# Optimization experiments

Hardware: AMD Instinct MI355X
Metric: run time of the kernel (lower is better)

The kernel has to match this reference:

```python
import jax, jax.numpy as jnp
import numpy as np

N = 50000   # nodes
E = 800000  # edges
D = 128     # att_dim
H = 8       # heads
DH = D // H # head dim
EPS = 1e-5


def _ln(x, g, b):
    m = jnp.mean(x, axis=-1, keepdims=True)
    v = jnp.mean((x - m) ** 2, axis=-1, keepdims=True)
    return (x - m) * jax.lax.rsqrt(v + EPS) * g + b


def setup_inputs() -> dict:
    key = jax.random.key(0)
    ks = jax.random.split(key, 12)
    s = 1.0 / np.sqrt(D)
    w = lambda k, sh: (jax.random.normal(k, sh, jnp.float32) * s)
    return {
        'x': jax.random.normal(ks[0], (N, D), jnp.float32),
        'idx_i': jax.random.randint(ks[1], (E,), 0, N, jnp.int32),
        'idx_j': jax.random.randint(ks[2], (E,), 0, N, jnp.int32),
        'Wq': w(ks[3], (D, D)), 'bq': jnp.zeros((D,), jnp.float32),
        'Wk': w(ks[4], (D, D)), 'bk': jnp.zeros((D,), jnp.float32),
        'Wv': w(ks[5], (D, D)), 'bv': jnp.zeros((D,), jnp.float32),
        'Wo': w(ks[6], (D, D)), 'bo': jnp.zeros((D,), jnp.float32),
        'g1': jnp.ones((D,), jnp.float32), 'be1': jnp.zeros((D,), jnp.float32),
        'W1': w(ks[7], (D, D)), 'bb1': jnp.zeros((D,), jnp.float32),
        'W2': w(ks[8], (D, D)), 'bb2': jnp.zeros((D,), jnp.float32),
        'g2': jnp.ones((D,), jnp.float32), 'be2': jnp.zeros((D,), jnp.float32),
    }


def reference(x, idx_i, idx_j, Wq, bq, Wk, bk, Wv, bv, Wo, bo,
              g1, be1, W1, bb1, W2, bb2, g2, be2):
    # --- EdgeAttentionLayer: multi-head dot-product attention over edges ---
    q = (x @ Wq + bq).reshape(N, H, DH)   # n h d
    k = (x @ Wk + bk).reshape(N, H, DH)
    v = (x @ Wv + bv).reshape(N, H, DH)
    q_i = q[idx_i]                         # (E, H, DH) gather at destination
    k_j = k[idx_j]                         # (E, H, DH) gather at source
    e = jnp.einsum('ehd,ehd->eh', q_i, k_j) / np.sqrt(DH)  # (E, H)
    # segment softmax over edges sharing the same destination node idx_i
    m = jax.ops.segment_max(e, idx_i, num_segments=N)       # (N, H)
    a = jnp.exp(e - m[idx_i])
    denom = jax.ops.segment_sum(a, idx_i, num_segments=N)   # (N, H)
    alpha = a / denom[idx_i]                                 # (E, H)
    agg = jax.ops.segment_sum(alpha[:, :, None] * v[idx_j], idx_i,
                              num_segments=N)                # (N, H, DH)
    x1 = agg.reshape(N, D) @ Wo + bo
    # --- residual + LayerNorm ---
    h = _ln(x + x1, g1, be1)
    # --- ResLayer projection: Linear -> ReLU -> Linear, residual, LayerNorm ---
    y = jax.nn.relu(h @ W1 + bb1) @ W2 + bb2
    return _ln(h + y, g2, be2)
```

## Files before the change

kernel.cpp:

```cpp
#include <hip/hip_runtime.h>
#include <hip/hip_bf16.h>
#include <math.h>

#define D 128
#define H 8
#define DH 16
#define SCAN_CHUNK 1024

typedef __attribute__((ext_vector_type(8))) short bf16x8;
typedef __attribute__((ext_vector_type(4))) float f32x4;

__device__ __forceinline__ float bf2f(ushort u) {
    unsigned int x = ((unsigned int)u) << 16;
    float f;
    __builtin_memcpy(&f, &x, 4);
    return f;
}
__device__ __forceinline__ ushort f2bf(float f) {
    __hip_bfloat16 h = __float2bfloat16(f);
    ushort u;
    __builtin_memcpy(&u, &h, 2);
    return u;
}

#define STAGE_W(SRC, LDSBUF)                                              \
    {                                                                      \
        _Pragma("unroll")                                                  \
        for (int it_ = 0; it_ < 8; ++it_) {                                \
            int idx16_ = t + it_ * 256;                                    \
            int row_ = idx16_ >> 4, c16_ = idx16_ & 15;                    \
            int d_ = (row_ << 7) + ((c16_ ^ (row_ & 7)) << 3);             \
            *(bf16x8*)((LDSBUF) + d_) = *(const bf16x8*)((SRC) + idx16_ * 8); \
        }                                                                  \
    }

#define WOFF(rn, kk) (((rn) << 7) + ((((l4) + (kk) * 4) ^ ((rn) & 7)) << 3))

#define LOAD_A(SRCH, SRCL, BASE, AH, AL)                                   \
    _Pragma("unroll")                                                      \
    for (int kk_ = 0; kk_ < 4; ++kk_) {                                    \
        AH[kk_] = *(const bf16x8*)((SRCH) + (BASE) + kk_ * 32);            \
        AL[kk_] = *(const bf16x8*)((SRCL) + (BASE) + kk_ * 32);            \
    }

#define TILE_MFMA(AH0, AL0, AH1, AL1, WH, WL, ACC0, ACC1)                  \
    _Pragma("unroll")                                                      \
    for (int kk = 0; kk < 4; ++kk) {                                       \
        _Pragma("unroll")                                                  \
        for (int n = 0; n < 8; ++n) {                                      \
            int rn = n * 16 + l15;                                         \
            bf16x8 bh = *(const bf16x8*)((WH) + WOFF(rn, kk));             \
            bf16x8 bl = *(const bf16x8*)((WL) + WOFF(rn, kk));             \
            ACC0[n] = __builtin_amdgcn_mfma_f32_16x16x32_bf16(AH0[kk], bh, ACC0[n], 0, 0, 0); \
            ACC0[n] = __builtin_amdgcn_mfma_f32_16x16x32_bf16(AL0[kk], bh, ACC0[n], 0, 0, 0); \
            ACC0[n] = __builtin_amdgcn_mfma_f32_16x16x32_bf16(AH0[kk], bl, ACC0[n], 0, 0, 0); \
            ACC1[n] = __builtin_amdgcn_mfma_f32_16x16x32_bf16(AH1[kk], bh, ACC1[n], 0, 0, 0); \
            ACC1[n] = __builtin_amdgcn_mfma_f32_16x16x32_bf16(AL1[kk], bh, ACC1[n], 0, 0, 0); \
            ACC1[n] = __builtin_amdgcn_mfma_f32_16x16x32_bf16(AH1[kk], bl, ACC1[n], 0, 0, 0); \
        }                                                                  \
    }


__global__ __launch_bounds__(256) void zero_kernel(int* __restrict__ count, int n) {
    int gid = blockIdx.x * blockDim.x + threadIdx.x;
    if (gid < n) count[gid] = 0;
}


__global__ __launch_bounds__(256) void prep_x_kernel(
    const float* __restrict__ x, ushort* __restrict__ xh, ushort* __restrict__ xl,
    int total4)
{
    int gid = blockIdx.x * blockDim.x + threadIdx.x;
    if (gid >= total4) return;
    float4 v = ((const float4*)x)[gid];
    ushort4 hv, lv;
    hv.x = f2bf(v.x); lv.x = f2bf(v.x - bf2f(hv.x));
    hv.y = f2bf(v.y); lv.y = f2bf(v.y - bf2f(hv.y));
    hv.z = f2bf(v.z); lv.z = f2bf(v.z - bf2f(hv.z));
    hv.w = f2bf(v.w); lv.w = f2bf(v.w - bf2f(hv.w));
    ((ushort4*)xh)[gid] = hv;
    ((ushort4*)xl)[gid] = lv;
}


__global__ __launch_bounds__(256) void prep_w_kernel(
    const float* __restrict__ w0, const float* __restrict__ w1,
    const float* __restrict__ w2, const float* __restrict__ w3,
    const float* __restrict__ w4, const float* __restrict__ w5,
    ushort* __restrict__ wth, ushort* __restrict__ wtl)
{
    __shared__ __align__(16) float tile[128][132];
    const int m = blockIdx.x;
    const float* W = (m == 0) ? w0 : (m == 1) ? w1 : (m == 2) ? w2
                   : (m == 3) ? w3 : (m == 4) ? w4 : w5;
    const int t = threadIdx.x;
    const float4* wg = (const float4*)W;
    #pragma unroll
    for (int it = 0; it < 16; ++it) {
        int f4 = t + it * 256;
        int k = f4 >> 5, c4 = f4 & 31;
        *((float4*)&tile[k][c4 * 4]) = wg[f4];
    }
    __syncthreads();
    ushort* oh = wth + m * 16384;
    ushort* ol = wtl + m * 16384;
    #pragma unroll
    for (int it = 0; it < 64; ++it) {
        int idx = t + it * 256;
        int c = idx >> 7, k = idx & 127;
        float v = tile[k][c];
        ushort hb = f2bf(v);
        oh[idx] = hb;
        ol[idx] = f2bf(v - bf2f(hb));
    }
}


__global__ __launch_bounds__(256) void gemm_qkv_kernel(
    const ushort* __restrict__ xh, const ushort* __restrict__ xl,
    const ushort* __restrict__ wth, const ushort* __restrict__ wtl,
    const float* __restrict__ bq, const float* __restrict__ bk,
    const float* __restrict__ bv,
    float* __restrict__ q, ushort* __restrict__ k16, ushort* __restrict__ v16,
    int n_rows)
{
    __shared__ __align__(16) ushort wh[16384];
    __shared__ __align__(16) ushort wl[16384];
    const int t = threadIdx.x;
    const int w = t >> 6, l = t & 63;
    const int l15 = l & 15, l4 = l >> 4;
    const int m = blockIdx.y;

    STAGE_W(wth + m * 16384, wh);
    STAGE_W(wtl + m * 16384, wl);

    const float* bias = (m == 0) ? bq : (m == 1) ? bk : bv;
    float bsv[8];
    #pragma unroll
    for (int n = 0; n < 8; ++n) bsv[n] = bias[n * 16 + l15];
    __syncthreads();

    const int ntiles = (n_rows + 127) >> 7;
    for (int tile = blockIdx.x; tile < ntiles; tile += gridDim.x) {
        const int rowb = tile * 128 + w * 32;
        const size_t a0 = (size_t)(rowb + l15) * D + l4 * 8;
        bf16x8 ah0[4], al0[4], ah1[4], al1[4];
        LOAD_A(xh, xl, a0, ah0, al0);
        LOAD_A(xh, xl, a0 + 16 * D, ah1, al1);
        f32x4 acc0[8], acc1[8];
        #pragma unroll
        for (int n = 0; n < 8; ++n) {
            acc0[n] = (f32x4){0.f, 0.f, 0.f, 0.f};
            acc1[n] = (f32x4){0.f, 0.f, 0.f, 0.f};
        }
        TILE_MFMA(ah0, al0, ah1, al1, wh, wl, acc0, acc1);
        #pragma unroll
        for (int n = 0; n < 8; ++n) {
            int col = n * 16 + l15;
            #pragma unroll
            for (int r = 0; r < 4; ++r) {
                int row0 = rowb + l4 * 4 + r;
                int row1 = row0 + 16;
                if (row0 < n_rows) {
                    float val = acc0[n][r] + bsv[n];
                    if (m == 0) q[(size_t)row0 * D + col] = val;
                    else if (m == 1) k16[(size_t)row0 * D + col] = f2bf(val);
                    else v16[(size_t)row0 * D + col] = f2bf(val);
                }
                if (row1 < n_rows) {
                    float val = acc1[n][r] + bsv[n];
                    if (m == 0) q[(size_t)row1 * D + col] = val;
                    else if (m == 1) k16[(size_t)row1 * D + col] = f2bf(val);
                    else v16[(size_t)row1 * D + col] = f2bf(val);
                }
            }
        }
    }
}


__global__ __launch_bounds__(256) void hist_kernel(
    const int* __restrict__ idx_i, int* __restrict__ count, int n_edges)
{
    int e = blockIdx.x * blockDim.x + threadIdx.x;
    if (e < n_edges) atomicAdd(&count[idx_i[e]], 1);
}

__global__ __launch_bounds__(256) void scan_reduce_kernel(
    const int* __restrict__ count, int* __restrict__ bsum, int n)
{
    __shared__ int wsum[4];
    const int t = threadIdx.x, lane = t & 63, w = t >> 6;
    int base = blockIdx.x * SCAN_CHUNK + t * 4;
    int s = 0;
    #pragma unroll
    for (int i = 0; i < 4; ++i) {
        int idx = base + i;
        if (idx < n) s += count[idx];
    }
    #pragma unroll
    for (int off = 1; off < 64; off <<= 1) s += __shfl_xor(s, off);
    if (lane == 0) wsum[w] = s;
    __syncthreads();
    if (t == 0) bsum[blockIdx.x] = wsum[0] + wsum[1] + wsum[2] + wsum[3];
}

__global__ __launch_bounds__(64) void scan_bsum_kernel(
    int* __restrict__ bsum, int* __restrict__ row_start, int nb, int n)
{
    const int t = threadIdx.x;
    int iv = (t < nb) ? bsum[t] : 0;
    int vv = iv;
    #pragma unroll
    for (int off = 1; off < 64; off <<= 1) {
        int u = __shfl_up(vv, off);
        if (t >= off) vv += u;
    }
    if (t < nb) bsum[t] = vv - iv;
    if (t == 63) row_start[n] = vv;
}

__global__ __launch_bounds__(256) void scan_write_kernel(
    const int* __restrict__ count, const int* __restrict__ bsum,
    int* __restrict__ row_start, int* __restrict__ cursor, int n)
{
    __shared__ int wtot[4];
    const int t = threadIdx.x, lane = t & 63, w = t >> 6;
    int base = blockIdx.x * SCAN_CHUNK + t * 4;
    int c0 = 0, c1 = 0, c2 = 0, c3 = 0;
    if (base + 0 < n) c0 = count[base + 0];
    if (base + 1 < n) c1 = count[base + 1];
    if (base + 2 < n) c2 = count[base + 2];
    if (base + 3 < n) c3 = count[base + 3];
    int tsum = c0 + c1 + c2 + c3;
    int inc = tsum;
    #pragma unroll
    for (int off = 1; off < 64; off <<= 1) {
        int u = __shfl_up(inc, off);
        if (lane >= off) inc += u;
    }
    if (lane == 63) wtot[w] = inc;
    __syncthreads();
    int wb = 0;
    for (int i = 0; i < w; ++i) wb += wtot[i];
    int start = bsum[blockIdx.x] + wb + inc - tsum;
    if (base + 0 < n) { row_start[base + 0] = start;            cursor[base + 0] = start; }
    if (base + 1 < n) { row_start[base + 1] = start + c0;       cursor[base + 1] = start + c0; }
    if (base + 2 < n) { row_start[base + 2] = start + c0 + c1;  cursor[base + 2] = start + c0 + c1; }
    if (base + 3 < n) { row_start[base + 3] = start + c0 + c1 + c2; cursor[base + 3] = start + c0 + c1 + c2; }
}

__global__ __launch_bounds__(256) void scatter_kernel(
    const int* __restrict__ idx_i, const int* __restrict__ idx_j,
    int* __restrict__ cursor, int* __restrict__ ejs, int n_edges)
{
    int e = blockIdx.x * blockDim.x + threadIdx.x;
    if (e < n_edges) {
        int i = idx_i[e];
        int pos = atomicAdd(&cursor[i], 1);
        ejs[pos] = idx_j[e];
    }
}


__global__ __launch_bounds__(256) void fused_agg_kernel(
    const float* __restrict__ q, const ushort* __restrict__ k16,
    const ushort* __restrict__ v16, const int* __restrict__ row_start,
    const int* __restrict__ ejs,
    ushort* __restrict__ aggh, ushort* __restrict__ aggl, int n_nodes)
{
    const int lane = threadIdx.x & 63;
    const int node = (blockIdx.x * blockDim.x + threadIdx.x) >> 6;
    if (node >= n_nodes) return;
    const int beg = row_start[node], end = row_start[node + 1];
    const int half = lane >> 5, sl = lane & 31;
    const int c4 = sl * 4;

    if (beg >= end) {
        if (half == 0) {
            ((uint2*)(aggh + (size_t)node * D))[sl] = make_uint2(0u, 0u);
            ((uint2*)(aggl + (size_t)node * D))[sl] = make_uint2(0u, 0u);
        }
        return;
    }

    const float4 qv = *(const float4*)&q[(size_t)node * D + c4];
    const float SC = 0.25f * 1.4426950408889634f;
    float m = -INFINITY, l = 0.f;
    float a0 = 0.f, a1 = 0.f, a2 = 0.f, a3 = 0.f;

    int p = beg + half;
    uint2 kr0, vr0, kr1, vr1;
    if (p < end) {
        int j = ejs[p];
        kr0 = *(const uint2*)(k16 + (size_t)j * D + c4);
        vr0 = *(const uint2*)(v16 + (size_t)j * D + c4);
    }
    if (p + 2 < end) {
        int j = ejs[p + 2];
        kr1 = *(const uint2*)(k16 + (size_t)j * D + c4);
        vr1 = *(const uint2*)(v16 + (size_t)j * D + c4);
    }
    while (p < end) {
        uint2 kc = kr0, vc = vr0;
        kr0 = kr1; vr0 = vr1;
        if (p + 4 < end) {
            int j = ejs[p + 4];
            kr1 = *(const uint2*)(k16 + (size_t)j * D + c4);
            vr1 = *(const uint2*)(v16 + (size_t)j * D + c4);
        }
        float k0 = bf2f((ushort)kc.x), k1 = bf2f((ushort)(kc.x >> 16));
        float k2 = bf2f((ushort)kc.y), k3 = bf2f((ushort)(kc.y >> 16));
        float d = qv.x * k0 + qv.y * k1 + qv.z * k2 + qv.w * k3;
        d += __shfl_xor(d, 1);
        d += __shfl_xor(d, 2);
        float s = d * SC;
        float mn = fmaxf(m, s);
        float c  = exp2f(m - mn);
        float pe = exp2f(s - mn);
        float v0 = bf2f((ushort)vc.x), v1 = bf2f((ushort)(vc.x >> 16));
        float v2 = bf2f((ushort)vc.y), v3 = bf2f((ushort)(vc.y >> 16));
        l  = l  * c + pe;
        a0 = a0 * c + pe * v0;
        a1 = a1 * c + pe * v1;
        a2 = a2 * c + pe * v2;
        a3 = a3 * c + pe * v3;
        m = mn;
        p += 2;
    }

    float m2 = __shfl_xor(m, 32);
    float l2 = __shfl_xor(l, 32);
    float b0 = __shfl_xor(a0, 32);
    float b1 = __shfl_xor(a1, 32);
    float b2 = __shfl_xor(a2, 32);
    float b3 = __shfl_xor(a3, 32);
    float mm = fmaxf(m, m2);
    float cA = exp2f(m - mm);
    float cB = exp2f(m2 - mm);
    float L  = l * cA + l2 * cB;
    float A0 = a0 * cA + b0 * cB;
    float A1 = a1 * cA + b1 * cB;
    float A2 = a2 * cA + b2 * cB;
    float A3 = a3 * cA + b3 * cB;
    float invl = (L > 0.f) ? (1.0f / L) : 0.f;
    float o0 = A0 * invl, o1 = A1 * invl, o2 = A2 * invl, o3 = A3 * invl;

    ushort h0 = f2bf(o0), h1 = f2bf(o1), h2 = f2bf(o2), h3 = f2bf(o3);
    if (half == 0) {
        uint2 hv;
        hv.x = (unsigned int)h0 | ((unsigned int)h1 << 16);
        hv.y = (unsigned int)h2 | ((unsigned int)h3 << 16);
        ((uint2*)(aggh + (size_t)node * D))[sl] = hv;
    } else {
        ushort l0 = f2bf(o0 - bf2f(h0)), l1 = f2bf(o1 - bf2f(h1));
        ushort l2_ = f2bf(o2 - bf2f(h2)), l3 = f2bf(o3 - bf2f(h3));
        uint2 lv;
        lv.x = (unsigned int)l0 | ((unsigned int)l1 << 16);
        lv.y = (unsigned int)l2_ | ((unsigned int)l3 << 16);
        ((uint2*)(aggl + (size_t)node * D))[sl] = lv;
    }
}


__global__ __launch_bounds__(256) void gemm_oproj_kernel(
    const ushort* __restrict__ aggh, const ushort* __restrict__ aggl,
    const float* __restrict__ x,
    const ushort* __restrict__ wth, const ushort* __restrict__ wtl,
    const float* __restrict__ bo, const float* __restrict__ g1,
    const float* __restrict__ be1,
    ushort* __restrict__ hh, ushort* __restrict__ hl, int n_rows)
{
    __shared__ __align__(16) ushort wh[16384];
    __shared__ __align__(16) ushort wl[16384];
    const int t = threadIdx.x;
    const int w = t >> 6, l = t & 63;
    const int l15 = l & 15, l4 = l >> 4;

    STAGE_W(wth, wh);
    STAGE_W(wtl, wl);
    float bsv[8], gv[8], bev[8];
    #pragma unroll
    for (int n = 0; n < 8; ++n) {
        int col = n * 16 + l15;
        bsv[n] = bo[col]; gv[n] = g1[col]; bev[n] = be1[col];
    }
    __syncthreads();

    const int ntiles = (n_rows + 127) >> 7;
    for (int tile = blockIdx.x; tile < ntiles; tile += gridDim.x) {
        const int rowb = tile * 128 + w * 32;
        const size_t a0 = (size_t)(rowb + l15) * D + l4 * 8;
        bf16x8 ah0[4], al0[4], ah1[4], al1[4];
        LOAD_A(aggh, aggl, a0, ah0, al0);
        LOAD_A(aggh, aggl, a0 + 16 * D, ah1, al1);
        f32x4 acc0[8], acc1[8];
        #pragma unroll
        for (int n = 0; n < 8; ++n) {
            acc0[n] = (f32x4){0.f, 0.f, 0.f, 0.f};
            acc1[n] = (f32x4){0.f, 0.f, 0.f, 0.f};
        }
        TILE_MFMA(ah0, al0, ah1, al1, wh, wl, acc0, acc1);
        #pragma unroll
        for (int g = 0; g < 2; ++g) {
            f32x4* acc = g ? acc1 : acc0;
            int rbase = rowb + g * 16;
            float vals[8][4];
            #pragma unroll
            for (int n = 0; n < 8; ++n) {
                int col = n * 16 + l15;
                #pragma unroll
                for (int r = 0; r < 4; ++r) {
                    int row = rbase + l4 * 4 + r;
                    float xr = (row < n_rows) ? x[(size_t)row * D + col] : 0.f;
                    vals[n][r] = acc[n][r] + bsv[n] + xr;
                }
            }
            #pragma unroll
            for (int r = 0; r < 4; ++r) {
                int row = rbase + l4 * 4 + r;
                float s = 0.f, ss = 0.f;
                #pragma unroll
                for (int n = 0; n < 8; ++n) { s += vals[n][r]; ss += vals[n][r] * vals[n][r]; }
                #pragma unroll
                for (int msk = 1; msk <= 8; msk <<= 1) {
                    s += __shfl_xor(s, msk);
                    ss += __shfl_xor(ss, msk);
                }
                float mean = s * (1.0f / D);
                float var = ss * (1.0f / D) - mean * mean;
                float inv = rsqrtf(var + 1e-5f);
                if (row < n_rows) {
                    #pragma unroll
                    for (int n = 0; n < 8; ++n) {
                        int col = n * 16 + l15;
                        float y = (vals[n][r] - mean) * inv * gv[n] + bev[n];
                        ushort hb = f2bf(y);
                        hh[(size_t)row * D + col] = hb;
                        hl[(size_t)row * D + col] = f2bf(y - bf2f(hb));
                    }
                }
            }
        }
    }
}


__global__ __launch_bounds__(256) void gemm_ffn1_kernel(
    const ushort* __restrict__ hh, const ushort* __restrict__ hl,
    const ushort* __restrict__ wth, const ushort* __restrict__ wtl,
    const float* __restrict__ bb1,
    ushort* __restrict__ th, ushort* __restrict__ tl, int n_rows)
{
    __shared__ __align__(16) ushort wh[16384];
    __shared__ __align__(16) ushort wl[16384];
    const int t = threadIdx.x;
    const int w = t >> 6, l = t & 63;
    const int l15 = l & 15, l4 = l >> 4;

    STAGE_W(wth, wh);
    STAGE_W(wtl, wl);
    float bsv[8];
    #pragma unroll
    for (int n = 0; n < 8; ++n) bsv[n] = bb1[n * 16 + l15];
    __syncthreads();

    const int ntiles = (n_rows + 127) >> 7;
    for (int tile = blockIdx.x; tile < ntiles; tile += gridDim.x) {
        const int rowb = tile * 128 + w * 32;
        const size_t a0 = (size_t)(rowb + l15) * D + l4 * 8;
        bf16x8 ah0[4], al0[4], ah1[4], al1[4];
        LOAD_A(hh, hl, a0, ah0, al0);
        LOAD_A(hh, hl, a0 + 16 * D, ah1, al1);
        f32x4 acc0[8], acc1[8];
        #pragma unroll
        for (int n = 0; n < 8; ++n) {
            acc0[n] = (f32x4){0.f, 0.f, 0.f, 0.f};
            acc1[n] = (f32x4){0.f, 0.f, 0.f, 0.f};
        }
        TILE_MFMA(ah0, al0, ah1, al1, wh, wl, acc0, acc1);
        #pragma unroll
        for (int n = 0; n < 8; ++n) {
            int col = n * 16 + l15;
            #pragma unroll
            for (int r = 0; r < 4; ++r) {
                int row0 = rowb + l4 * 4 + r;
                int row1 = row0 + 16;
                if (row0 < n_rows) {
                    float tv = fmaxf(acc0[n][r] + bsv[n], 0.f);
                    ushort hb = f2bf(tv);
                    th[(size_t)row0 * D + col] = hb;
                    tl[(size_t)row0 * D + col] = f2bf(tv - bf2f(hb));
                }
                if (row1 < n_rows) {
                    float tv = fmaxf(acc1[n][r] + bsv[n], 0.f);
                    ushort hb = f2bf(tv);
                    th[(size_t)row1 * D + col] = hb;
                    tl[(size_t)row1 * D + col] = f2bf(tv - bf2f(hb));
                }
            }
        }
    }
}


__global__ __launch_bounds__(256) void gemm_ffn2_kernel(
    const ushort* __restrict__ th, const ushort* __restrict__ tl,
    const ushort* __restrict__ hh, const ushort* __restrict__ hl,
    const ushort* __restrict__ wth, const ushort* __restrict__ wtl,
    const float* __restrict__ bb2, const float* __restrict__ g2,
    const float* __restrict__ be2,
    float* __restrict__ out, int n_rows)
{
    __shared__ __align__(16) ushort wh[16384];
    __shared__ __align__(16) ushort wl[16384];
    const int t = threadIdx.x;
    const int w = t >> 6, l = t & 63;
    const int l15 = l & 15, l4 = l >> 4;

    STAGE_W(wth, wh);
    STAGE_W(wtl, wl);
    float bsv[8], gv[8], bev[8];
    #pragma unroll
    for (int n = 0; n < 8; ++n) {
        int col = n * 16 + l15;
        bsv[n] = bb2[col]; gv[n] = g2[col]; bev[n] = be2[col];
    }
    __syncthreads();

    const int ntiles = (n_rows + 127) >> 7;
    for (int tile = blockIdx.x; tile < ntiles; tile += gridDim.x) {
        const int rowb = tile * 128 + w * 32;
        const size_t a0 = (size_t)(rowb + l15) * D + l4 * 8;
        bf16x8 ah0[4], al0[4], ah1[4], al1[4];
        LOAD_A(th, tl, a0, ah0, al0);
        LOAD_A(th, tl, a0 + 16 * D, ah1, al1);
        f32x4 acc0[8], acc1[8];
        #pragma unroll
        for (int n = 0; n < 8; ++n) {
            acc0[n] = (f32x4){0.f, 0.f, 0.f, 0.f};
            acc1[n] = (f32x4){0.f, 0.f, 0.f, 0.f};
        }
        TILE_MFMA(ah0, al0, ah1, al1, wh, wl, acc0, acc1);
        #pragma unroll
        for (int g = 0; g < 2; ++g) {
            f32x4* acc = g ? acc1 : acc0;
            int rbase = rowb + g * 16;
            float vals[8][4];
            #pragma unroll
            for (int n = 0; n < 8; ++n) {
                int col = n * 16 + l15;
                #pragma unroll
                for (int r = 0; r < 4; ++r) {
                    int row = rbase + l4 * 4 + r;
                    float hr = 0.f;
                    if (row < n_rows)
                        hr = bf2f(hh[(size_t)row * D + col]) + bf2f(hl[(size_t)row * D + col]);
                    vals[n][r] = acc[n][r] + bsv[n] + hr;
                }
            }
            #pragma unroll
            for (int r = 0; r < 4; ++r) {
                int row = rbase + l4 * 4 + r;
                float s = 0.f, ss = 0.f;
                #pragma unroll
                for (int n = 0; n < 8; ++n) { s += vals[n][r]; ss += vals[n][r] * vals[n][r]; }
                #pragma unroll
                for (int msk = 1; msk <= 8; msk <<= 1) {
                    s += __shfl_xor(s, msk);
                    ss += __shfl_xor(ss, msk);
                }
                float mean = s * (1.0f / D);
                float var = ss * (1.0f / D) - mean * mean;
                float inv = rsqrtf(var + 1e-5f);
                if (row < n_rows) {
                    #pragma unroll
                    for (int n = 0; n < 8; ++n) {
                        int col = n * 16 + l15;
                        out[(size_t)row * D + col] = (vals[n][r] - mean) * inv * gv[n] + bev[n];
                    }
                }
            }
        }
    }
}


extern "C" void kernel_launch(void* const* d_in, const int* in_sizes, int n_in,
                              void* d_out, int out_size, void* d_ws, size_t ws_size,
                              hipStream_t stream) {
    const float* x     = (const float*)d_in[0];
    const int*   idx_i = (const int*)d_in[1];
    const int*   idx_j = (const int*)d_in[2];
    const float* Wq = (const float*)d_in[3];
    const float* bq = (const float*)d_in[4];
    const float* Wk = (const float*)d_in[5];
    const float* bk = (const float*)d_in[6];
    const float* Wv = (const float*)d_in[7];
    const float* bv = (const float*)d_in[8];
    const float* Wo = (const float*)d_in[9];
    const float* bo = (const float*)d_in[10];
    const float* g1 = (const float*)d_in[11];
    const float* be1 = (const float*)d_in[12];
    const float* W1 = (const float*)d_in[13];
    const float* bb1 = (const float*)d_in[14];
    const float* W2 = (const float*)d_in[15];
    const float* bb2 = (const float*)d_in[16];
    const float* g2 = (const float*)d_in[17];
    const float* be2 = (const float*)d_in[18];

    const int N_ = in_sizes[0] / D;
    const int E_ = in_sizes[1];
    const size_t ND = (size_t)N_ * D;
    const int nb = (N_ + SCAN_CHUNK - 1) / SCAN_CHUNK;

    float* ws = (float*)d_ws;
    float* q = ws;
    ushort* k16 = (ushort*)(q + ND);
    ushort* v16 = k16 + ND;
    int* count     = (int*)(v16 + ND);
    int* row_start = count + N_;
    int* cursor    = row_start + N_ + 1;
    int* bsum      = cursor + N_;
    int* ejs       = bsum + 64;
    ushort* xh = (ushort*)(ejs + E_);
    ushort* xl = xh + ND;
    ushort* wth = xl + ND;
    ushort* wtl = wth + 6 * 16384;
    ushort* aggh = xh;
    ushort* aggl = xl;
    ushort* hh = (ushort*)q;
    ushort* hl = hh + ND;
    ushort* th = k16;
    ushort* tl = v16;

    zero_kernel<<<(N_ + 255) / 256, 256, 0, stream>>>(count, N_);
    prep_x_kernel<<<((int)(ND / 4) + 255) / 256, 256, 0, stream>>>(x, xh, xl, (int)(ND / 4));
    prep_w_kernel<<<6, 256, 0, stream>>>(Wq, Wk, Wv, Wo, W1, W2, wth, wtl);
    {
        dim3 g(171, 3);
        gemm_qkv_kernel<<<g, 256, 0, stream>>>(xh, xl, wth, wtl,
                                               bq, bk, bv, q, k16, v16, N_);
    }
    hist_kernel<<<(E_ + 255) / 256, 256, 0, stream>>>(idx_i, count, E_);
    scan_reduce_kernel<<<nb, 256, 0, stream>>>(count, bsum, N_);
    scan_bsum_kernel<<<1, 64, 0, stream>>>(bsum, row_start, nb, N_);
    scan_write_kernel<<<nb, 256, 0, stream>>>(count, bsum, row_start, cursor, N_);
    scatter_kernel<<<(E_ + 255) / 256, 256, 0, stream>>>(idx_i, idx_j, cursor, ejs, E_);
    fused_agg_kernel<<<(N_ + 3) / 4, 256, 0, stream>>>(q, k16, v16, row_start, ejs,
                                                       aggh, aggl, N_);
    gemm_oproj_kernel<<<196, 256, 0, stream>>>(aggh, aggl, x,
                                               wth + 3 * 16384, wtl + 3 * 16384,
                                               bo, g1, be1, hh, hl, N_);
    gemm_ffn1_kernel<<<196, 256, 0, stream>>>(hh, hl,
                                              wth + 4 * 16384, wtl + 4 * 16384,
                                              bb1, th, tl, N_);
    gemm_ffn2_kernel<<<196, 256, 0, stream>>>(th, tl, hh, hl,
                                              wth + 5 * 16384, wtl + 5 * 16384,
                                              bb2, g2, be2, (float*)d_out, N_);
}
```

Measured before the change: 291.8 us.

## Double-buffer A fragments in GEMMs and add lazy softmax rescaling in aggregation

All four split-bf16 GEMM kernels now prefetch the next tile's A fragments into a second register set while computing the current tile, hiding global load latency. Each also gets __launch_bounds__(256,2), and the QKV grid shrinks from 171 to 131 blocks per matrix. The aggregation kernel pre-scales q and skips the online-softmax rescale unless some lane's score exceeds the running max by more than 8 (log2 units), turning most updates into plain FMAs. The extra fragment registers raise register pressure, and the lazy max lets exponent terms grow by up to 2^8 before rescaling.

Measured after the change: 414.1 us. 41.9% more time.

```diff
diff --git a/kernel.cpp b/kernel.cpp
--- a/kernel.cpp
+++ b/kernel.cpp
@@ -34,31 +34,48 @@
         }                                                                  \
     }
 
-#define WOFF(rn, kk) (((rn) << 7) + ((((l4) + (kk) * 4) ^ ((rn) & 7)) << 3))
-
-#define LOAD_A(SRCH, SRCL, BASE, AH, AL)                                   \
-    _Pragma("unroll")                                                      \
-    for (int kk_ = 0; kk_ < 4; ++kk_) {                                    \
-        AH[kk_] = *(const bf16x8*)((SRCH) + (BASE) + kk_ * 32);            \
-        AL[kk_] = *(const bf16x8*)((SRCL) + (BASE) + kk_ * 32);            \
-    }
-
-#define TILE_MFMA(AH0, AL0, AH1, AL1, WH, WL, ACC0, ACC1)                  \
-    _Pragma("unroll")                                                      \
-    for (int kk = 0; kk < 4; ++kk) {                                       \
+#define DECL_FRAGS(P) bf16x8 P##h0[4], P##l0[4], P##h1[4], P##l1[4]
+
+#define LOAD_FRAGS(SRCH, SRCL, TILE, P)                                    \
+    {                                                                      \
+        const int rb_ = (TILE) * 128 + w * 32;                             \
+        const size_t a0_ = (size_t)(rb_ + l15) * D + l4 * 8;               \
         _Pragma("unroll")                                                  \
-        for (int n = 0; n < 8; ++n) {                                      \
-            int rn = n * 16 + l15;                                         \
-            bf16x8 bh = *(const bf16x8*)((WH) + WOFF(rn, kk));             \
-            bf16x8 bl = *(const bf16x8*)((WL) + WOFF(rn, kk));             \
-            ACC0[n] = __builtin_amdgcn_mfma_f32_16x16x32_bf16(AH0[kk], bh, ACC0[n], 0, 0, 0); \
-            ACC0[n] = __builtin_amdgcn_mfma_f32_16x16x32_bf16(AL0[kk], bh, ACC0[n], 0, 0, 0); \
-            ACC0[n] = __builtin_amdgcn_mfma_f32_16x16x32_bf16(AH0[kk], bl, ACC0[n], 0, 0, 0); \
-            ACC1[n] = __builtin_amdgcn_mfma_f32_16x16x32_bf16(AH1[kk], bh, ACC1[n], 0, 0, 0); \
-            ACC1[n] = __builtin_amdgcn_mfma_f32_16x16x32_bf16(AL1[kk], bh, ACC1[n], 0, 0, 0); \
-            ACC1[n] = __builtin_amdgcn_mfma_f32_16x16x32_bf16(AH1[kk], bl, ACC1[n], 0, 0, 0); \
+        for (int kk_ = 0; kk_ < 4; ++kk_) {                                \
+            P##h0[kk_] = *(const bf16x8*)((SRCH) + a0_ + kk_ * 32);        \
+            P##l0[kk_] = *(const bf16x8*)((SRCL) + a0_ + kk_ * 32);        \
+            P##h1[kk_] = *(const bf16x8*)((SRCH) + a0_ + 16 * D + kk_ * 32); \
+            P##l1[kk_] = *(const bf16x8*)((SRCL) + a0_ + 16 * D + kk_ * 32); \
         }                                                                  \
     }
+
+__device__ __forceinline__ f32x4 MFMA(bf16x8 a, bf16x8 b, f32x4 c) {
+    return __builtin_amdgcn_mfma_f32_16x16x32_bf16(a, b, c, 0, 0, 0);
+}
+
+__device__ __forceinline__ void tile_mfma(
+    const bf16x8* ah0, const bf16x8* al0,
+    const bf16x8* ah1, const bf16x8* al1,
+    const ushort* wh, const ushort* wl, int l15, int l4,
+    f32x4* acc0, f32x4* acc1)
+{
+    #pragma unroll
+    for (int kk = 0; kk < 4; ++kk) {
+        #pragma unroll
+        for (int n = 0; n < 8; ++n) {
+            int rn = n * 16 + l15;
+            int off = (rn << 7) + (((l4 + kk * 4) ^ (rn & 7)) << 3);
+            bf16x8 bh = *(const bf16x8*)(wh + off);
+            bf16x8 bl = *(const bf16x8*)(wl + off);
+            acc0[n] = MFMA(ah0[kk], bh, acc0[n]);
+            acc0[n] = MFMA(al0[kk], bh, acc0[n]);
+            acc0[n] = MFMA(ah0[kk], bl, acc0[n]);
+            acc1[n] = MFMA(ah1[kk], bh, acc1[n]);
+            acc1[n] = MFMA(al1[kk], bh, acc1[n]);
+            acc1[n] = MFMA(ah1[kk], bl, acc1[n]);
+        }
+    }
+}
 
 
 __global__ __launch_bounds__(256) void zero_kernel(int* __restrict__ count, int n) {
@@ -117,7 +134,39 @@
 }
 
 
-__global__ __launch_bounds__(256) void gemm_qkv_kernel(
+#define QKV_ITER(TILE, P)                                                  \
+    {                                                                      \
+        f32x4 acc0[8], acc1[8];                                            \
+        _Pragma("unroll")                                                  \
+        for (int n = 0; n < 8; ++n) {                                      \
+            acc0[n] = (f32x4){0.f, 0.f, 0.f, 0.f};                         \
+            acc1[n] = (f32x4){0.f, 0.f, 0.f, 0.f};                         \
+        }                                                                  \
+        tile_mfma(P##h0, P##l0, P##h1, P##l1, wh, wl, l15, l4, acc0, acc1);\
+        const int rowb_ = (TILE) * 128 + w * 32;                           \
+        _Pragma("unroll")                                                  \
+        for (int n = 0; n < 8; ++n) {                                      \
+            int col = n * 16 + l15;                                        \
+            _Pragma("unroll")                                              \
+            for (int r = 0; r < 4; ++r) {                                  \
+                int row0 = rowb_ + l4 * 4 + r, row1 = row0 + 16;           \
+                if (row0 < n_rows) {                                       \
+                    float val = acc0[n][r] + bsv[n];                       \
+                    if (mat == 0) q[(size_t)row0 * D + col] = val;         \
+                    else if (mat == 1) k16[(size_t)row0 * D + col] = f2bf(val); \
+                    else v16[(size_t)row0 * D + col] = f2bf(val);          \
+                }                                                          \
+                if (row1 < n_rows) {                                       \
+                    float val = acc1[n][r] + bsv[n];                       \
+                    if (mat == 0) q[(size_t)row1 * D + col] = val;         \
+                    else if (mat == 1) k16[(size_t)row1 * D + col] = f2bf(val); \
+                    else v16[(size_t)row1 * D + col] = f2bf(val);          \
+                }                                                          \
+            }                                                              \
+        }                                                                  \
+    }
+
+__global__ __launch_bounds__(256, 2) void gemm_qkv_kernel(
     const ushort* __restrict__ xh, const ushort* __restrict__ xl,
     const ushort* __restrict__ wth, const ushort* __restrict__ wtl,
     const float* __restrict__ bq, const float* __restrict__ bk,
@@ -130,52 +179,34 @@
     const int t = threadIdx.x;
     const int w = t >> 6, l = t & 63;
     const int l15 = l & 15, l4 = l >> 4;
-    const int m = blockIdx.y;
-
-    STAGE_W(wth + m * 16384, wh);
-    STAGE_W(wtl + m * 16384, wl);
-
-    const float* bias = (m == 0) ? bq : (m == 1) ? bk : bv;
+    const int mat = blockIdx.y;
+
+    STAGE_W(wth + mat * 16384, wh);
+    STAGE_W(wtl + mat * 16384, wl);
+    const float* bias = (mat == 0) ? bq : (mat == 1) ? bk : bv;
     float bsv[8];
     #pragma unroll
     for (int n = 0; n < 8; ++n) bsv[n] = bias[n * 16 + l15];
     __syncthreads();
 
     const int ntiles = (n_rows + 127) >> 7;
-    for (int tile = blockIdx.x; tile < ntiles; tile += gridDim.x) {
-        const int rowb = tile * 128 + w * 32;
-        const size_t a0 = (size_t)(rowb + l15) * D + l4 * 8;
-        bf16x8 ah0[4], al0[4], ah1[4], al1[4];
-        LOAD_A(xh, xl, a0, ah0, al0);
-        LOAD_A(xh, xl, a0 + 16 * D, ah1, al1);
-        f32x4 acc0[8], acc1[8];
-        #pragma unroll
-        for (int n = 0; n < 8; ++n) {
-            acc0[n] = (f32x4){0.f, 0.f, 0.f, 0.f};
-            acc1[n] = (f32x4){0.f, 0.f, 0.f, 0.f};
-        }
-        TILE_MFMA(ah0, al0, ah1, al1, wh, wl, acc0, acc1);
-        #pragma unroll
-        for (int n = 0; n < 8; ++n) {
-            int col = n * 16 + l15;
-            #pragma unroll
-            for (int r = 0; r < 4; ++r) {
-                int row0 = rowb + l4 * 4 + r;
-                int row1 = row0 + 16;
-                if (row0 < n_rows) {
-                    float val = acc0[n][r] + bsv[n];
-                    if (m == 0) q[(size_t)row0 * D + col] = val;
-                    else if (m == 1) k16[(size_t)row0 * D + col] = f2bf(val);
-                    else v16[(size_t)row0 * D + col] = f2bf(val);
-                }
-                if (row1 < n_rows) {
-                    float val = acc1[n][r] + bsv[n];
-                    if (m == 0) q[(size_t)row1 * D + col] = val;
-                    else if (m == 1) k16[(size_t)row1 * D + col] = f2bf(val);
-                    else v16[(size_t)row1 * D + col] = f2bf(val);
-                }
-            }
-        }
+    const int g = gridDim.x;
+    int tile = blockIdx.x;
+    if (tile >= ntiles) return;
+
+    DECL_FRAGS(pA);
+    DECL_FRAGS(pB);
+    LOAD_FRAGS(xh, xl, tile, pA);
+    for (;;) {
+        int n1 = tile + g;
+        if (n1 < ntiles) LOAD_FRAGS(xh, xl, n1, pB);
+        QKV_ITER(tile, pA);
+        if (n1 >= ntiles) break;
+        int n2 = n1 + g;
+        if (n2 < ntiles) LOAD_FRAGS(xh, xl, n2, pA);
+        QKV_ITER(n1, pB);
+        if (n2 >= ntiles) break;
+        tile = n2;
     }
 }
 
@@ -285,8 +316,9 @@
         return;
     }
 
-    const float4 qv = *(const float4*)&q[(size_t)node * D + c4];
     const float SC = 0.25f * 1.4426950408889634f;
+    float4 qv = *(const float4*)&q[(size_t)node * D + c4];
+    qv.x *= SC; qv.y *= SC; qv.z *= SC; qv.w *= SC;
     float m = -INFINITY, l = 0.f;
     float a0 = 0.f, a1 = 0.f, a2 = 0.f, a3 = 0.f;
 
@@ -312,21 +344,29 @@
         }
         float k0 = bf2f((ushort)kc.x), k1 = bf2f((ushort)(kc.x >> 16));
         float k2 = bf2f((ushort)kc.y), k3 = bf2f((ushort)(kc.y >> 16));
-        float d = qv.x * k0 + qv.y * k1 + qv.z * k2 + qv.w * k3;
-        d += __shfl_xor(d, 1);
-        d += __shfl_xor(d, 2);
-        float s = d * SC;
-        float mn = fmaxf(m, s);
-        float c  = exp2f(m - mn);
-        float pe = exp2f(s - mn);
+        float s = qv.x * k0 + qv.y * k1 + qv.z * k2 + qv.w * k3;
+        s += __shfl_xor(s, 1);
+        s += __shfl_xor(s, 2);
         float v0 = bf2f((ushort)vc.x), v1 = bf2f((ushort)(vc.x >> 16));
         float v2 = bf2f((ushort)vc.y), v3 = bf2f((ushort)(vc.y >> 16));
-        l  = l  * c + pe;
-        a0 = a0 * c + pe * v0;
-        a1 = a1 * c + pe * v1;
-        a2 = a2 * c + pe * v2;
-        a3 = a3 * c + pe * v3;
-        m = mn;
+        if (__any(s > m + 8.f)) {
+            float mn = fmaxf(m, s);
+            float c  = exp2f(m - mn);
+            float pe = exp2f(s - mn);
+            l  = l  * c + pe;
+            a0 = a0 * c + pe * v0;
+            a1 = a1 * c + pe * v1;
+            a2 = a2 * c + pe * v2;
+            a3 = a3 * c + pe * v3;
+            m = mn;
+        } else {
+            float pe = exp2f(s - m);
+            l += pe;
+            a0 = fmaf(pe, v0, a0);
+            a1 = fmaf(pe, v1, a1);
+            a2 = fmaf(pe, v2, a2);
+            a3 = fmaf(pe, v3, a3);
+        }
         p += 2;
     }
 
@@ -364,7 +404,65 @@
 }
 
 
-__global__ __launch_bounds__(256) void gemm_oproj_kernel(
+__device__ __forceinline__ void oproj_epi(
+    const f32x4* acc, int rbase, int l15, int l4,
+    const float* __restrict__ x, const float* bsv, const float* gv,
+    const float* bev, ushort* __restrict__ hh, ushort* __restrict__ hl,
+    int n_rows)
+{
+    float vals[8][4];
+    #pragma unroll
+    for (int n = 0; n < 8; ++n) {
+        int col = n * 16 + l15;
+        #pragma unroll
+        for (int r = 0; r < 4; ++r) {
+            int row = rbase + l4 * 4 + r;
+            float xr = (row < n_rows) ? x[(size_t)row * D + col] : 0.f;
+            vals[n][r] = acc[n][r] + bsv[n] + xr;
+        }
+    }
+    #pragma unroll
+    for (int r = 0; r < 4; ++r) {
+        int row = rbase + l4 * 4 + r;
+        float s = 0.f, ss = 0.f;
+        #pragma unroll
+        for (int n = 0; n < 8; ++n) { s += vals[n][r]; ss += vals[n][r] * vals[n][r]; }
+        #pragma unroll
+        for (int msk = 1; msk <= 8; msk <<= 1) {
+            s += __shfl_xor(s, msk);
+            ss += __shfl_xor(ss, msk);
+        }
+        float mean = s * (1.0f / D);
+        float var = ss * (1.0f / D) - mean * mean;
+        float inv = rsqrtf(var + 1e-5f);
+        if (row < n_rows) {
+            #pragma unroll
+            for (int n = 0; n < 8; ++n) {
+                int col = n * 16 + l15;
+                float y = (vals[n][r] - mean) * inv * gv[n] + bev[n];
+                ushort hb = f2bf(y);
+                hh[(size_t)row * D + col] = hb;
+                hl[(size_t)row * D + col] = f2bf(y - bf2f(hb));
+            }
+        }
+    }
+}
+
+#define OPROJ_ITER(TILE, P)                                                \
+    {                                                                      \
+        f32x4 acc0[8], acc1[8];                                            \
+        _Pragma("unroll")                                                  \
+        for (int n = 0; n < 8; ++n) {                                      \
+            acc0[n] = (f32x4){0.f, 0.f, 0.f, 0.f};                         \
+            acc1[n] = (f32x4){0.f, 0.f, 0.f, 0.f};                         \
+        }                                                                  \
+        tile_mfma(P##h0, P##l0, P##h1, P##l1, wh, wl, l15, l4, acc0, acc1);\
+        const int rowb_ = (TILE) * 128 + w * 32;                           \
+        oproj_epi(acc0, rowb_,      l15, l4, x, bsv, gv, bev, hh, hl, n_rows); \
+        oproj_epi(acc1, rowb_ + 16, l15, l4, x, bsv, gv, bev, hh, hl, n_rows); \
+    }
+
+__global__ __launch_bounds__(256, 2) void gemm_oproj_kernel(
     const ushort* __restrict__ aggh, const ushort* __restrict__ aggl,
     const float* __restrict__ x,
     const ushort* __restrict__ wth, const ushort* __restrict__ wtl,
@@ -389,65 +487,60 @@
     __syncthreads();
 
     const int ntiles = (n_rows + 127) >> 7;
-    for (int tile = blockIdx.x; tile < ntiles; tile += gridDim.x) {
-        const int rowb = tile * 128 + w * 32;
-        const size_t a0 = (size_t)(rowb + l15) * D + l4 * 8;
-        bf16x8 ah0[4], al0[4], ah1[4], al1[4];
-        LOAD_A(aggh, aggl, a0, ah0, al0);
-        LOAD_A(aggh, aggl, a0 + 16 * D, ah1, al1);
-        f32x4 acc0[8], acc1[8];
-        #pragma unroll
-        for (int n = 0; n < 8; ++n) {
-            acc0[n] = (f32x4){0.f, 0.f, 0.f, 0.f};
-            acc1[n] = (f32x4){0.f, 0.f, 0.f, 0.f};
-        }
-        TILE_MFMA(ah0, al0, ah1, al1, wh, wl, acc0, acc1);
-        #pragma unroll
-        for (int g = 0; g < 2; ++g) {
-            f32x4* acc = g ? acc1 : acc0;
-            int rbase = rowb + g * 16;
-            float vals[8][4];
-            #pragma unroll
-            for (int n = 0; n < 8; ++n) {
-                int col = n * 16 + l15;
-                #pragma unroll
-                for (int r = 0; r < 4; ++r) {
-                    int row = rbase + l4 * 4 + r;
-                    float xr = (row < n_rows) ? x[(size_t)row * D + col] : 0.f;
-                    vals[n][r] = acc[n][r] + bsv[n] + xr;
-                }
-            }
-            #pragma unroll
-            for (int r = 0; r < 4; ++r) {
-                int row = rbase + l4 * 4 + r;
-                float s = 0.f, ss = 0.f;
-                #pragma unroll
-                for (int n = 0; n < 8; ++n) { s += vals[n][r]; ss += vals[n][r] * vals[n][r]; }
-                #pragma unroll
-                for (int msk = 1; msk <= 8; msk <<= 1) {
-                    s += __shfl_xor(s, msk);
-                    ss += __shfl_xor(ss, msk);
-                }
-                float mean = s * (1.0f / D);
-                float var = ss * (1.0f / D) - mean * mean;
-                float inv = rsqrtf(var + 1e-5f);
-                if (row < n_rows) {
-                    #pragma unroll
-                    for (int n = 0; n < 8; ++n) {
-                        int col = n * 16 + l15;
-                        float y = (vals[n][r] - mean) * inv * gv[n] + bev[n];
-                        ushort hb = f2bf(y);
-                        hh[(size_t)row * D + col] = hb;
-                        hl[(size_t)row * D + col] = f2bf(y - bf2f(hb));
-                    }
-                }
-            }
-        }
-    }
-}
-
-
-__global__ __launch_bounds__(256) void gemm_ffn1_kernel(
+    const int g = gridDim.x;
+    int tile = blockIdx.x;
+    if (tile >= ntiles) return;
+
+    DECL_FRAGS(pA);
+    DECL_FRAGS(pB);
+    LOAD_FRAGS(aggh, aggl, tile, pA);
+    for (;;) {
+        int n1 = tile + g;
+        if (n1 < ntiles) LOAD_FRAGS(aggh, aggl, n1, pB);
+        OPROJ_ITER(tile, pA);
+        if (n1 >= ntiles) break;
+        int n2 = n1 + g;
+        if (n2 < ntiles) LOAD_FRAGS(aggh, aggl, n2, pA);
+        OPROJ_ITER(n1, pB);
+        if (n2 >= ntiles) break;
+        tile = n2;
+    }
+}
+
+
+#define FFN1_ITER(TILE, P)                                                 \
+    {                                                                      \
+        f32x4 acc0[8], acc1[8];                                            \
+        _Pragma("unroll")                                                  \
+        for (int n = 0; n < 8; ++n) {                                      \
+            acc0[n] = (f32x4){0.f, 0.f, 0.f, 0.f};                         \
+            acc1[n] = (f32x4){0.f, 0.f, 0.f, 0.f};                         \
+        }                                                                  \
+        tile_mfma(P##h0, P##l0, P##h1, P##l1, wh, wl, l15, l4, acc0, acc1);\
+        const int rowb_ = (TILE) * 128 + w * 32;                           \
+        _Pragma("unroll")                                                  \
+        for (int n = 0; n < 8; ++n) {                                      \
+            int col = n * 16 + l15;                                        \
+            _Pragma("unroll")                                              \
+            for (int r = 0; r < 4; ++r) {                                  \
+                int row0 = rowb_ + l4 * 4 + r, row1 = row0 + 16;           \
+                if (row0 < n_rows) {                                       \
+                    float tv = fmaxf(acc0[n][r] + bsv[n], 0.f);            \
+                    ushort hb = f2bf(tv);                                  \
+                    th[(size_t)row0 * D + col] = hb;                       \
+                    tl[(size_t)row0 * D + col] = f2bf(tv - bf2f(hb));      \
+                }                                                          \
+                if (row1 < n_rows) {                                       \
+                    float tv = fmaxf(acc1[n][r] + bsv[n], 0.f);            \
+                    ushort hb = f2bf(tv);                                  \
+                    th[(size_t)row1 * D + col] = hb;                       \
+                    tl[(size_t)row1 * D + col] = f2bf(tv - bf2f(hb));      \
+                }                                                          \
+            }                                                              \
+        }                                                                  \
+    }
+
+__global__ __launch_bounds__(256, 2) void gemm_ffn1_kernel(
     const ushort* __restrict__ hh, const ushort* __restrict__ hl,
     const ushort* __restrict__ wth, const ushort* __restrict__ wtl,
     const float* __restrict__ bb1,
@@ -467,45 +560,85 @@
     __syncthreads();
 
     const int ntiles = (n_rows + 127) >> 7;
-    for (int tile = blockIdx.x; tile < ntiles; tile += gridDim.x) {
-        const int rowb = tile * 128 + w * 32;
-        const size_t a0 = (size_t)(rowb + l15) * D + l4 * 8;
-        bf16x8 ah0[4], al0[4], ah1[4], al1[4];
-        LOAD_A(hh, hl, a0, ah0, al0);
-        LOAD_A(hh, hl, a0 + 16 * D, ah1, al1);
-        f32x4 acc0[8], acc1[8];
+    const int g = gridDim.x;
+    int tile = blockIdx.x;
+    if (tile >= ntiles) return;
+
+    DECL_FRAGS(pA);
+    DECL_FRAGS(pB);
+    LOAD_FRAGS(hh, hl, tile, pA);
+    for (;;) {
+        int n1 = tile + g;
+        if (n1 < ntiles) LOAD_FRAGS(hh, hl, n1, pB);
+        FFN1_ITER(tile, pA);
+        if (n1 >= ntiles) break;
+        int n2 = n1 + g;
+        if (n2 < ntiles) LOAD_FRAGS(hh, hl, n2, pA);
+        FFN1_ITER(n1, pB);
+        if (n2 >= ntiles) break;
+        tile = n2;
+    }
+}
+
+
+__device__ __forceinline__ void ffn2_epi(
+    const f32x4* acc, int rbase, int l15, int l4,
+    const ushort* __restrict__ hh, const ushort* __restrict__ hl,
+    const float* bsv, const float* gv, const float* bev,
+    float* __restrict__ out, int n_rows)
+{
+    float vals[8][4];
+    #pragma unroll
+    for (int n = 0; n < 8; ++n) {
+        int col = n * 16 + l15;
         #pragma unroll
-        for (int n = 0; n < 8; ++n) {
-            acc0[n] = (f32x4){0.f, 0.f, 0.f, 0.f};
-            acc1[n] = (f32x4){0.f, 0.f, 0.f, 0.f};
-        }
-        TILE_MFMA(ah0, al0, ah1, al1, wh, wl, acc0, acc1);
+        for (int r = 0; r < 4; ++r) {
+            int row = rbase + l4 * 4 + r;
+            float hr = 0.f;
+            if (row < n_rows)
+                hr = bf2f(hh[(size_t)row * D + col]) + bf2f(hl[(size_t)row * D + col]);
+            vals[n][r] = acc[n][r] + bsv[n] + hr;
+        }
+    }
+    #pragma unroll
+    for (int r = 0; r < 4; ++r) {
+        int row = rbase + l4 * 4 + r;
+        float s = 0.f, ss = 0.f;
         #pragma unroll
-        for (int n = 0; n < 8; ++n) {
-            int col = n * 16 + l15;
+        for (int n = 0; n < 8; ++n) { s += vals[n][r]; ss += vals[n][r] * vals[n][r]; }
+        #pragma unroll
+        for (int msk = 1; msk <= 8; msk <<= 1) {
+            s += __shfl_xor(s, msk);
+            ss += __shfl_xor(ss, msk);
+        }
+        float mean = s * (1.0f / D);
+        float var = ss * (1.0f / D) - mean * mean;
+        float inv = rsqrtf(var + 1e-5f);
+        if (row < n_rows) {
             #pragma unroll
-            for (int r = 0; r < 4; ++r) {
-                int row0 = rowb + l4 * 4 + r;
-                int row1 = row0 + 16;
-                if (row0 < n_rows) {
-                    float tv = fmaxf(acc0[n][r] + bsv[n], 0.f);
-                    ushort hb = f2bf(tv);
-                    th[(size_t)row0 * D + col] = hb;
-                    tl[(size_t)row0 * D + col] = f2bf(tv - bf2f(hb));
-                }
-                if (row1 < n_rows) {
-                    float tv = fmaxf(acc1[n][r] + bsv[n], 0.f);
-                    ushort hb = f2bf(tv);
-                    th[(size_t)row1 * D + col] = hb;
-                    tl[(size_t)row1 * D + col] = f2bf(tv - bf2f(hb));
-                }
+            for (int n = 0; n < 8; ++n) {
+                int col = n * 16 + l15;
+                out[(size_t)row * D + col] = (vals[n][r] - mean) * inv * gv[n] + bev[n];
             }
         }
     }
 }
 
-
-__global__ __launch_bounds__(256) void gemm_ffn2_kernel(
+#define FFN2_ITER(TILE, P)                                                 \
+    {                                                                      \
+        f32x4 acc0[8], acc1[8];                                            \
+        _Pragma("unroll")                                                  \
+        for (int n = 0; n < 8; ++n) {                                      \
+            acc0[n] = (f32x4){0.f, 0.f, 0.f, 0.f};                         \
+            acc1[n] = (f32x4){0.f, 0.f, 0.f, 0.f};                         \
+        }                                                                  \
+        tile_mfma(P##h0, P##l0, P##h1, P##l1, wh, wl, l15, l4, acc0, acc1);\
+        const int rowb_ = (TILE) * 128 + w * 32;                           \
+        ffn2_epi(acc0, rowb_,      l15, l4, hh, hl, bsv, gv, bev, out, n_rows); \
+        ffn2_epi(acc1, rowb_ + 16, l15, l4, hh, hl, bsv, gv, bev, out, n_rows); \
+    }
+
+__global__ __launch_bounds__(256, 2) void gemm_ffn2_kernel(
     const ushort* __restrict__ th, const ushort* __restrict__ tl,
     const ushort* __restrict__ hh, const ushort* __restrict__ hl,
     const ushort* __restrict__ wth, const ushort* __restrict__ wtl,
@@ -530,59 +663,23 @@
     __syncthreads();
 
     const int ntiles = (n_rows + 127) >> 7;
-    for (int tile = blockIdx.x; tile < ntiles; tile += gridDim.x) {
-        const int rowb = tile * 128 + w * 32;
-        const size_t a0 = (size_t)(rowb + l15) * D + l4 * 8;
-        bf16x8 ah0[4], al0[4], ah1[4], al1[4];
-        LOAD_A(th, tl, a0, ah0, al0);
-        LOAD_A(th, tl, a0 + 16 * D, ah1, al1);
-        f32x4 acc0[8], acc1[8];
-        #pragma unroll
-        for (int n = 0; n < 8; ++n) {
-            acc0[n] = (f32x4){0.f, 0.f, 0.f, 0.f};
-            acc1[n] = (f32x4){0.f, 0.f, 0.f, 0.f};
-        }
-        TILE_MFMA(ah0, al0, ah1, al1, wh, wl, acc0, acc1);
-        #pragma unroll
-        for (int g = 0; g < 2; ++g) {
-            f32x4* acc = g ? acc1 : acc0;
-            int rbase = rowb + g * 16;
-            float vals[8][4];
-            #pragma unroll
-            for (int n = 0; n < 8; ++n) {
-                int col = n * 16 + l15;
-                #pragma unroll
-                for (int r = 0; r < 4; ++r) {
-                    int row = rbase + l4 * 4 + r;
-                    float hr = 0.f;
-                    if (row < n_rows)
-                        hr = bf2f(hh[(size_t)row * D + col]) + bf2f(hl[(size_t)row * D + col]);
-                    vals[n][r] = acc[n][r] + bsv[n] + hr;
-                }
-            }
-            #pragma unroll
-            for (int r = 0; r < 4; ++r) {
-                int row = rbase + l4 * 4 + r;
-                float s = 0.f, ss = 0.f;
-                #pragma unroll
-                for (int n = 0; n < 8; ++n) { s += vals[n][r]; ss += vals[n][r] * vals[n][r]; }
-                #pragma unroll
-                for (int msk = 1; msk <= 8; msk <<= 1) {
-                    s += __shfl_xor(s, msk);
-                    ss += __shfl_xor(ss, msk);
-                }
-                float mean = s * (1.0f / D);
-                float var = ss * (1.0f / D) - mean * mean;
-                float inv = rsqrtf(var + 1e-5f);
-                if (row < n_rows) {
-                    #pragma unroll
-                    for (int n = 0; n < 8; ++n) {
-                        int col = n * 16 + l15;
-                        out[(size_t)row * D + col] = (vals[n][r] - mean) * inv * gv[n] + bev[n];
-                    }
-                }
-            }
-        }
+    const int g = gridDim.x;
+    int tile = blockIdx.x;
+    if (tile >= ntiles) return;
+
+    DECL_FRAGS(pA);
+    DECL_FRAGS(pB);
+    LOAD_FRAGS(th, tl, tile, pA);
+    for (;;) {
+        int n1 = tile + g;
+        if (n1 < ntiles) LOAD_FRAGS(th, tl, n1, pB);
+        FFN2_ITER(tile, pA);
+        if (n1 >= ntiles) break;
+        int n2 = n1 + g;
+        if (n2 < ntiles) LOAD_FRAGS(th, tl, n2, pA);
+        FFN2_ITER(n1, pB);
+        if (n2 >= ntiles) break;
+        tile = n2;
     }
 }
 
@@ -639,7 +736,7 @@
     prep_x_kernel<<<((int)(ND / 4) + 255) / 256, 256, 0, stream>>>(x, xh, xl, (int)(ND / 4));
     prep_w_kernel<<<6, 256, 0, stream>>>(Wq, Wk, Wv, Wo, W1, W2, wth, wtl);
     {
-        dim3 g(171, 3);
+        dim3 g(131, 3);
         gemm_qkv_kernel<<<g, 256, 0, stream>>>(xh, xl, wth, wtl,
                                                bq, bk, bv, q, k16, v16, N_);
     }
```
